# Performance work log

Measured on AMD Instinct MI355X. Metric: run time of the kernel, lower is better.

The kernel has to match this reference:

```python
import jax, jax.numpy as jnp
import numpy as np

N_NODES = 100000
N_EDGES = 1600000
HIDDEN = 128
N_FILTERS = 64
CUTOFF = 8.0
BN_EPS = 1e-3  # keras BatchNormalization default epsilon


def setup_inputs() -> dict:
    key = jax.random.key(0)
    ks = jax.random.split(key, 12)
    x = jax.random.normal(ks[0], (N_NODES, HIDDEN), dtype=jnp.float32)
    edge_index = jax.random.randint(ks[1], (2, N_EDGES), 0, N_NODES, dtype=jnp.int32)
    edge_weight = jax.random.uniform(ks[2], (N_EDGES,), dtype=jnp.float32) * CUTOFF
    edge_attr = jax.random.uniform(ks[3], (N_EDGES, 1), dtype=jnp.float32)
    s = 0.05
    # filter_net: Dense(1->64, tanh), Dense(64->64)
    Wf1 = jax.random.normal(ks[4], (1, N_FILTERS), dtype=jnp.float32) * s
    bf1 = jnp.zeros((N_FILTERS,), jnp.float32)
    Wf2 = jax.random.normal(ks[5], (N_FILTERS, N_FILTERS), dtype=jnp.float32) * s
    bf2 = jnp.zeros((N_FILTERS,), jnp.float32)
    # interaction_net: Dense(128->128, softplus), Dense(128->128)
    Wi1 = jax.random.normal(ks[6], (HIDDEN, HIDDEN), dtype=jnp.float32) * s
    bi1 = jnp.zeros((HIDDEN,), jnp.float32)
    Wi2 = jax.random.normal(ks[7], (HIDDEN, HIDDEN), dtype=jnp.float32) * s
    bi2 = jnp.zeros((HIDDEN,), jnp.float32)
    # BatchNormalization (inference: moving stats)
    gamma = jnp.ones((HIDDEN,), jnp.float32)
    beta = jnp.zeros((HIDDEN,), jnp.float32)
    mov_mean = jax.random.normal(ks[8], (HIDDEN,), dtype=jnp.float32) * 0.01
    mov_var = jnp.ones((HIDDEN,), jnp.float32)
    return {"x": x, "edge_index": edge_index, "edge_weight": edge_weight,
            "edge_attr": edge_attr, "Wf1": Wf1, "bf1": bf1, "Wf2": Wf2, "bf2": bf2,
            "Wi1": Wi1, "bi1": bi1, "Wi2": Wi2, "bi2": bi2,
            "gamma": gamma, "beta": beta, "mov_mean": mov_mean, "mov_var": mov_var}


def reference(x, edge_index, edge_weight, edge_attr, Wf1, bf1, Wf2, bf2,
              Wi1, bi1, Wi2, bi2, gamma, beta, mov_mean, mov_var):
    row, col = edge_index[0], edge_index[1]
    # continuous filters with smooth cosine cutoff
    scaled = edge_weight * (2.0 / CUTOFF) - 1.0                    # [E]
    h = jnp.tanh(scaled[:, None] @ Wf1 + bf1)                      # [E, F]
    filters = h @ Wf2 + bf2                                        # [E, F]
    cut = 0.5 * (jnp.cos(edge_weight * jnp.pi / CUTOFF) + 1.0)
    cut = jnp.where(edge_weight <= CUTOFF, cut, 0.0)               # [E]
    filters = filters * cut[:, None]
    # Original: (neighbor[:, None, :] * filters[:, :, None]).sum(axis=1)
    # == neighbor * filters.sum(-1, keepdims) — same math, no [E,F,H] tensor.
    fsum = jnp.sum(filters, axis=-1, keepdims=True)                # [E, 1]
    messages = x[col] * fsum                                       # [E, H]
    agg = jax.ops.segment_sum(messages, row, num_segments=x.shape[0])  # [N, H]
    out = jax.nn.softplus(agg @ Wi1 + bi1) @ Wi2 + bi2             # [N, H]
    # BatchNormalization, inference mode (training=False)
    out = gamma * (out - mov_mean) * jax.lax.rsqrt(mov_var + BN_EPS) + beta
    return out
```

## Files before the change

### kernel.cpp

```cpp
#include <hip/hip_runtime.h>
#include <math.h>

#define HIDDEN 128
#define NFILT 64
#define SCAN_B 1024
#define LUTK 2048

typedef __attribute__((ext_vector_type(8))) short bf16x8;
typedef __attribute__((ext_vector_type(4))) float f32x4;

__device__ __forceinline__ short f2bf(float f) {
    unsigned u = __float_as_uint(f);
    unsigned r = (u + 0x7fffu + ((u >> 16) & 1u)) >> 16;
    return (short)r;
}
__device__ __forceinline__ float bf2f(unsigned short u) {
    return __uint_as_float(((unsigned)u) << 16);
}

__global__ void wsum_kernel(const float* __restrict__ Wf2, const float* __restrict__ bf2,
                            float* __restrict__ wsum, float* __restrict__ bsum) {
    int j = threadIdx.x;
    float s = 0.f;
    for (int f = 0; f < NFILT; ++f) s += Wf2[j * NFILT + f];
    wsum[j] = s;
    if (j == 0) {
        float b = 0.f;
        for (int f = 0; f < NFILT; ++f) b += bf2[f];
        *bsum = b;
    }
}

__device__ __forceinline__ float edge_coeff(float w,
                                            const float* sW, const float* sB,
                                            const float* sS, float bsum) {
    float s = fmaf(w, 0.25f, -1.0f);
    float acc = bsum;
    #pragma unroll 8
    for (int j = 0; j < NFILT; ++j)
        acc += tanhf(fmaf(s, sW[j], sB[j])) * sS[j];
    float cut = (w <= 8.0f) ? 0.5f * (cosf(w * 0.39269908169872414f) + 1.0f) : 0.0f;
    return acc * cut;
}

__global__ void lut_kernel(const float* __restrict__ Wf1, const float* __restrict__ bf1,
                           const float* __restrict__ wsum, const float* __restrict__ bsum,
                           float* __restrict__ lut) {
    int i = blockIdx.x * 256 + threadIdx.x;
    if (i > LUTK) return;
    float w = 8.0f * (float)i / (float)LUTK;
    lut[i] = edge_coeff(w, Wf1, bf1, wsum, *bsum);
}

__device__ __forceinline__ float lut_eval(const float* sl, float w) {
    float t = w * ((float)LUTK / 8.0f);
    t = fminf(fmaxf(t, 0.f), (float)LUTK);
    int i = (int)t;
    i = min(i, LUTK - 1);
    return fmaf(t - (float)i, sl[i + 1] - sl[i], sl[i]);
}

__global__ void prep_w_kernel(const float* __restrict__ Wi1, const float* __restrict__ Wi2,
                              short* __restrict__ W1T, short* __restrict__ W2T) {
    int idx = blockIdx.x * 256 + threadIdx.x;
    const float* src = (idx < 16384) ? Wi1 : Wi2;
    short* dst = (idx < 16384) ? W1T : W2T;
    int i = idx & 16383;
    int k = i >> 7, n = i & 127;
    dst[n * HIDDEN + k] = f2bf(src[i]);
}

__global__ void prep_bn_kernel(const float* __restrict__ bi2,
                               const float* __restrict__ gamma, const float* __restrict__ beta,
                               const float* __restrict__ mean, const float* __restrict__ var,
                               float* __restrict__ scf, float* __restrict__ shf) {
    int j = threadIdx.x;
    float sc = gamma[j] * rsqrtf(var[j] + 1e-3f);
    scf[j] = sc;
    shf[j] = (bi2[j] - mean[j]) * sc + beta[j];
}

__global__ void x2bf_kernel(const float* __restrict__ x, short* __restrict__ xh, int total8) {
    int i = blockIdx.x * 256 + threadIdx.x;
    if (i >= total8) return;
    const float4 v0 = *(const float4*)&x[(size_t)i * 8];
    const float4 v1 = *(const float4*)&x[(size_t)i * 8 + 4];
    bf16x8 o;
    o[0] = f2bf(v0.x); o[1] = f2bf(v0.y); o[2] = f2bf(v0.z); o[3] = f2bf(v0.w);
    o[4] = f2bf(v1.x); o[5] = f2bf(v1.y); o[6] = f2bf(v1.z); o[7] = f2bf(v1.w);
    *(bf16x8*)&xh[(size_t)i * 8] = o;
}

__global__ void count_rank_kernel(const int* __restrict__ rows, int* __restrict__ deg,
                                  int* __restrict__ rank, int E) {
    int e = blockIdx.x * blockDim.x + threadIdx.x;
    if (e < E) rank[e] = atomicAdd(&deg[rows[e]], 1);
}

__global__ void count_kernel(const int* __restrict__ rows, int* __restrict__ deg, int E) {
    int e = blockIdx.x * blockDim.x + threadIdx.x;
    if (e < E) atomicAdd(&deg[rows[e]], 1);
}

__global__ __launch_bounds__(SCAN_B) void scan_p1(const int* __restrict__ deg,
                                                  int* __restrict__ bsums, int N) {
    __shared__ int red[SCAN_B];
    int i = blockIdx.x * SCAN_B + threadIdx.x;
    red[threadIdx.x] = (i < N) ? deg[i] : 0;
    __syncthreads();
    for (int off = SCAN_B / 2; off > 0; off >>= 1) {
        if (threadIdx.x < off) red[threadIdx.x] += red[threadIdx.x + off];
        __syncthreads();
    }
    if (threadIdx.x == 0) bsums[blockIdx.x] = red[0];
}

__global__ __launch_bounds__(SCAN_B) void scan_p2(int* __restrict__ bsums, int B) {
    __shared__ int part[SCAN_B];
    int t = threadIdx.x;
    part[t] = (t < B) ? bsums[t] : 0;
    __syncthreads();
    for (int off = 1; off < SCAN_B; off <<= 1) {
        int v = (t >= off) ? part[t - off] : 0;
        __syncthreads();
        part[t] += v;
        __syncthreads();
    }
    if (t < B) bsums[t] = (t == 0) ? 0 : part[t - 1];
}

template <bool WRITE_CURSOR>
__global__ __launch_bounds__(SCAN_B) void scan_p3_t(int* __restrict__ deg,
                                                    const int* __restrict__ bsums,
                                                    int* __restrict__ offs, int N) {
    __shared__ int part[SCAN_B];
    int t = threadIdx.x;
    int i = blockIdx.x * SCAN_B + t;
    int d = (i < N) ? deg[i] : 0;
    part[t] = d;
    __syncthreads();
    for (int off = 1; off < SCAN_B; off <<= 1) {
        int v = (t >= off) ? part[t - off] : 0;
        __syncthreads();
        part[t] += v;
        __syncthreads();
    }
    int pre = bsums[blockIdx.x] + part[t] - d;
    if (i < N) {
        offs[i] = pre;
        if (WRITE_CURSOR) deg[i] = pre;
        if (i == N - 1) offs[N] = pre + d;
    }
}

__global__ __launch_bounds__(256) void fill_rank_kernel(
    const int* __restrict__ rows, const int* __restrict__ cols,
    const float* __restrict__ ew, const int* __restrict__ rank,
    const int* __restrict__ offs, const float* __restrict__ lut,
    int2* __restrict__ epack, int E) {
    __shared__ float sl[LUTK + 1];
    for (int i = threadIdx.x; i <= LUTK; i += 256) sl[i] = lut[i];
    __syncthreads();
    int e = blockIdx.x * 256 + threadIdx.x;
    if (e >= E) return;
    float f = lut_eval(sl, ew[e]);
    int pos = offs[rows[e]] + rank[e];
    epack[pos] = make_int2(cols[e], __float_as_int(f));
}

__global__ __launch_bounds__(256) void fill_cursor_kernel(
    const int* __restrict__ rows, const int* __restrict__ cols,
    const float* __restrict__ ew, int* __restrict__ cursor,
    const float* __restrict__ lut, int2* __restrict__ epack, int E) {
    __shared__ float sl[LUTK + 1];
    for (int i = threadIdx.x; i <= LUTK; i += 256) sl[i] = lut[i];
    __syncthreads();
    int e = blockIdx.x * 256 + threadIdx.x;
    if (e >= E) return;
    float f = lut_eval(sl, ew[e]);
    int pos = atomicAdd(&cursor[rows[e]], 1);
    epack[pos] = make_int2(cols[e], __float_as_int(f));
}

__global__ __launch_bounds__(256) void gather_bf_kernel(const int* __restrict__ offs,
                                                        const int2* __restrict__ epack,
                                                        const short* __restrict__ xh,
                                                        short* __restrict__ aggh, int N) {
    int t = threadIdx.x;
    int node = blockIdx.x * 8 + (t >> 5);
    if (node >= N) return;
    int lane = t & 31;
    int s = offs[node], eend = offs[node + 1];
    float a0 = 0.f, a1 = 0.f, a2 = 0.f, a3 = 0.f;

    int i = s;
    for (; i + 4 <= eend; i += 4) {
        int2 p0 = epack[i];
        int2 p1 = epack[i + 1];
        int2 p2 = epack[i + 2];
        int2 p3 = epack[i + 3];
        ushort4 x0 = *(const ushort4*)&xh[(size_t)p0.x * HIDDEN + lane * 4];
        ushort4 x1 = *(const ushort4*)&xh[(size_t)p1.x * HIDDEN + lane * 4];
        ushort4 x2 = *(const ushort4*)&xh[(size_t)p2.x * HIDDEN + lane * 4];
        ushort4 x3 = *(const ushort4*)&xh[(size_t)p3.x * HIDDEN + lane * 4];
        float f0 = __int_as_float(p0.y), f1 = __int_as_float(p1.y);
        float f2 = __int_as_float(p2.y), f3 = __int_as_float(p3.y);
        a0 = fmaf(bf2f(x0.x), f0, a0); a1 = fmaf(bf2f(x0.y), f0, a1);
        a2 = fmaf(bf2f(x0.z), f0, a2); a3 = fmaf(bf2f(x0.w), f0, a3);
        a0 = fmaf(bf2f(x1.x), f1, a0); a1 = fmaf(bf2f(x1.y), f1, a1);
        a2 = fmaf(bf2f(x1.z), f1, a2); a3 = fmaf(bf2f(x1.w), f1, a3);
        a0 = fmaf(bf2f(x2.x), f2, a0); a1 = fmaf(bf2f(x2.y), f2, a1);
        a2 = fmaf(bf2f(x2.z), f2, a2); a3 = fmaf(bf2f(x2.w), f2, a3);
        a0 = fmaf(bf2f(x3.x), f3, a0); a1 = fmaf(bf2f(x3.y), f3, a1);
        a2 = fmaf(bf2f(x3.z), f3, a2); a3 = fmaf(bf2f(x3.w), f3, a3);
    }
    for (; i < eend; ++i) {
        int2 p = epack[i];
        float f = __int_as_float(p.y);
        ushort4 xv = *(const ushort4*)&xh[(size_t)p.x * HIDDEN + lane * 4];
        a0 = fmaf(bf2f(xv.x), f, a0);
        a1 = fmaf(bf2f(xv.y), f, a1);
        a2 = fmaf(bf2f(xv.z), f, a2);
        a3 = fmaf(bf2f(xv.w), f, a3);
    }
    ushort4 o;
    o.x = (unsigned short)f2bf(a0);
    o.y = (unsigned short)f2bf(a1);
    o.z = (unsigned short)f2bf(a2);
    o.w = (unsigned short)f2bf(a3);
    *(ushort4*)&aggh[(size_t)node * HIDDEN + lane * 4] = o;
}

__global__ __launch_bounds__(256) void gather_kernel(const int* __restrict__ offs,
                                                     const int2* __restrict__ epack,
                                                     const float* __restrict__ x,
                                                     float* __restrict__ agg, int N) {
    int t = threadIdx.x;
    int node = blockIdx.x * 8 + (t >> 5);
    if (node >= N) return;
    int lane = t & 31;
    int s = offs[node], eend = offs[node + 1];
    float4 acc = make_float4(0.f, 0.f, 0.f, 0.f);
    int i = s;
    for (; i + 2 <= eend; i += 2) {
        int2 p0 = epack[i];
        int2 p1 = epack[i + 1];
        float4 x0 = *(const float4*)&x[(size_t)p0.x * HIDDEN + lane * 4];
        float4 x1 = *(const float4*)&x[(size_t)p1.x * HIDDEN + lane * 4];
        float f0 = __int_as_float(p0.y), f1 = __int_as_float(p1.y);
        acc.x = fmaf(x0.x, f0, acc.x); acc.y = fmaf(x0.y, f0, acc.y);
        acc.z = fmaf(x0.z, f0, acc.z); acc.w = fmaf(x0.w, f0, acc.w);
        acc.x = fmaf(x1.x, f1, acc.x); acc.y = fmaf(x1.y, f1, acc.y);
        acc.z = fmaf(x1.z, f1, acc.z); acc.w = fmaf(x1.w, f1, acc.w);
    }
    for (; i < eend; ++i) {
        int2 p = epack[i];
        float f = __int_as_float(p.y);
        const float4 xv = *(const float4*)&x[(size_t)p.x * HIDDEN + lane * 4];
        acc.x = fmaf(xv.x, f, acc.x);
        acc.y = fmaf(xv.y, f, acc.y);
        acc.z = fmaf(xv.z, f, acc.z);
        acc.w = fmaf(xv.w, f, acc.w);
    }
    *(float4*)&agg[(size_t)node * HIDDEN + lane * 4] = acc;
}

#define HROW 136

__global__ __launch_bounds__(256) void mlp_mfma_bf_kernel(
    const short* __restrict__ aggh, float* __restrict__ io,
    const short* __restrict__ W1T, const short* __restrict__ W2T,
    const float* __restrict__ bi1,
    const float* __restrict__ scf, const float* __restrict__ shf,
    int N) {
    __shared__ short hS[64 * HROW];

    const int t = threadIdx.x;
    const int wave = t >> 6;
    const int lane = t & 63;
    const int quad = lane >> 4;
    const int m16  = lane & 15;
    const int row0 = blockIdx.x * 64 + wave * 16;
    const int arow = row0 + m16;

    f32x4 acc[8];
    #pragma unroll
    for (int ct = 0; ct < 8; ++ct) acc[ct] = (f32x4)(0.f);

    #pragma unroll
    for (int ks = 0; ks < 4; ++ks) {
        bf16x8 a;
        if (arow < N) {
            a = *(const bf16x8*)&aggh[(size_t)arow * HIDDEN + ks * 32 + quad * 8];
        } else {
            #pragma unroll
            for (int j = 0; j < 8; ++j) a[j] = 0;
        }
        #pragma unroll
        for (int ct = 0; ct < 8; ++ct) {
            bf16x8 b = *(const bf16x8*)&W1T[(ct * 16 + m16) * HIDDEN + ks * 32 + quad * 8];
            acc[ct] = __builtin_amdgcn_mfma_f32_16x16x32_bf16(a, b, acc[ct], 0, 0, 0);
        }
    }

    #pragma unroll
    for (int ct = 0; ct < 8; ++ct) {
        int col = ct * 16 + m16;
        float b1 = bi1[col];
        #pragma unroll
        for (int r = 0; r < 4; ++r) {
            int lrow = wave * 16 + quad * 4 + r;
            float v = acc[ct][r] + b1;
            float h = (v > 20.f) ? v : log1pf(__expf(v));
            hS[lrow * HROW + col] = f2bf(h);
            acc[ct][r] = 0.f;
        }
    }
    __syncthreads();

    #pragma unroll
    for (int ks = 0; ks < 4; ++ks) {
        bf16x8 a = *(const bf16x8*)&hS[(wave * 16 + m16) * HROW + ks * 32 + quad * 8];
        #pragma unroll
        for (int ct = 0; ct < 8; ++ct) {
            bf16x8 b = *(const bf16x8*)&W2T[(ct * 16 + m16) * HIDDEN + ks * 32 + quad * 8];
            acc[ct] = __builtin_amdgcn_mfma_f32_16x16x32_bf16(a, b, acc[ct], 0, 0, 0);
        }
    }

    #pragma unroll
    for (int ct = 0; ct < 8; ++ct) {
        int col = ct * 16 + m16;
        float sc = scf[col], sh = shf[col];
        #pragma unroll
        for (int r = 0; r < 4; ++r) {
            int grow = row0 + quad * 4 + r;
            if (grow < N)
                io[(size_t)grow * HIDDEN + col] = fmaf(acc[ct][r], sc, sh);
        }
    }
}

__global__ __launch_bounds__(256) void mlp_mfma_kernel(
    float* io,
    const short* __restrict__ W1T, const short* __restrict__ W2T,
    const float* __restrict__ bi1,
    const float* __restrict__ scf, const float* __restrict__ shf,
    int N) {
    __shared__ short hS[64 * HROW];

    const int t = threadIdx.x;
    const int wave = t >> 6;
    const int lane = t & 63;
    const int quad = lane >> 4;
    const int m16  = lane & 15;
    const int row0 = blockIdx.x * 64 + wave * 16;
    const int arow = row0 + m16;

    f32x4 acc[8];
    #pragma unroll
    for (int ct = 0; ct < 8; ++ct) acc[ct] = (f32x4)(0.f);

    #pragma unroll
    for (int ks = 0; ks < 4; ++ks) {
        bf16x8 a;
        if (arow < N) {
            const float* ap = &io[(size_t)arow * HIDDEN + ks * 32 + quad * 8];
            float4 v0 = *(const float4*)ap;
            float4 v1 = *(const float4*)(ap + 4);
            a[0] = f2bf(v0.x); a[1] = f2bf(v0.y); a[2] = f2bf(v0.z); a[3] = f2bf(v0.w);
            a[4] = f2bf(v1.x); a[5] = f2bf(v1.y); a[6] = f2bf(v1.z); a[7] = f2bf(v1.w);
        } else {
            #pragma unroll
            for (int j = 0; j < 8; ++j) a[j] = 0;
        }
        #pragma unroll
        for (int ct = 0; ct < 8; ++ct) {
            bf16x8 b = *(const bf16x8*)&W1T[(ct * 16 + m16) * HIDDEN + ks * 32 + quad * 8];
            acc[ct] = __builtin_amdgcn_mfma_f32_16x16x32_bf16(a, b, acc[ct], 0, 0, 0);
        }
    }

    #pragma unroll
    for (int ct = 0; ct < 8; ++ct) {
        int col = ct * 16 + m16;
        float b1 = bi1[col];
        #pragma unroll
        for (int r = 0; r < 4; ++r) {
            int lrow = wave * 16 + quad * 4 + r;
            float v = acc[ct][r] + b1;
            float h = (v > 20.f) ? v : log1pf(__expf(v));
            hS[lrow * HROW + col] = f2bf(h);
            acc[ct][r] = 0.f;
        }
    }
    __syncthreads();

    #pragma unroll
    for (int ks = 0; ks < 4; ++ks) {
        bf16x8 a = *(const bf16x8*)&hS[(wave * 16 + m16) * HROW + ks * 32 + quad * 8];
        #pragma unroll
        for (int ct = 0; ct < 8; ++ct) {
            bf16x8 b = *(const bf16x8*)&W2T[(ct * 16 + m16) * HIDDEN + ks * 32 + quad * 8];
            acc[ct] = __builtin_amdgcn_mfma_f32_16x16x32_bf16(a, b, acc[ct], 0, 0, 0);
        }
    }

    #pragma unroll
    for (int ct = 0; ct < 8; ++ct) {
        int col = ct * 16 + m16;
        float sc = scf[col], sh = shf[col];
        #pragma unroll
        for (int r = 0; r < 4; ++r) {
            int grow = row0 + quad * 4 + r;
            if (grow < N)
                io[(size_t)grow * HIDDEN + col] = fmaf(acc[ct][r], sc, sh);
        }
    }
}

__global__ void edge_filter_kernel(const float* __restrict__ ew,
                                   const float* __restrict__ Wf1, const float* __restrict__ bf1,
                                   const float* __restrict__ wsum, const float* __restrict__ bsum,
                                   float* __restrict__ fs, int E) {
    __shared__ float sW[NFILT], sB[NFILT], sS[NFILT];
    if (threadIdx.x < NFILT) {
        sW[threadIdx.x] = Wf1[threadIdx.x];
        sB[threadIdx.x] = bf1[threadIdx.x];
        sS[threadIdx.x] = wsum[threadIdx.x];
    }
    __syncthreads();
    int e = blockIdx.x * blockDim.x + threadIdx.x;
    if (e >= E) return;
    fs[e] = edge_coeff(ew[e], sW, sB, sS, *bsum);
}

__global__ void scatter_kernel(const int* __restrict__ rows, const int* __restrict__ cols,
                               const float* __restrict__ x, const float* __restrict__ fs,
                               float* __restrict__ agg, int E) {
    int t = threadIdx.x;
    int e = blockIdx.x * 8 + (t >> 5);
    if (e >= E) return;
    int lane = t & 31;
    int r = rows[e];
    int c = cols[e];
    float f = fs[e];
    const float4 xv = *(const float4*)&x[c * HIDDEN + lane * 4];
    float* dst = &agg[r * HIDDEN + lane * 4];
    atomicAdd(dst + 0, xv.x * f);
    atomicAdd(dst + 1, xv.y * f);
    atomicAdd(dst + 2, xv.z * f);
    atomicAdd(dst + 3, xv.w * f);
}

__global__ __launch_bounds__(256) void mlp_kernel(
    float* __restrict__ io,
    const float* __restrict__ Wi1, const float* __restrict__ bi1,
    const float* __restrict__ Wi2, const float* __restrict__ bi2,
    const float* __restrict__ gamma, const float* __restrict__ beta,
    const float* __restrict__ mean, const float* __restrict__ var,
    int N) {
    __shared__ float As[64 * HIDDEN];
    __shared__ float Wh[64 * HIDDEN];

    const int t = threadIdx.x;
    const int row0 = blockIdx.x * 64;
    const int col4 = (t & 31) * 4;
    const int rgrp = t >> 5;

    #pragma unroll
    for (int i = 0; i < 8; ++i) {
        int f4 = t + 256 * i;
        int r = f4 >> 5, c4 = (f4 & 31) * 4;
        int node = row0 + r;
        float4 v = make_float4(0.f, 0.f, 0.f, 0.f);
        if (node < N) v = *(const float4*)&io[node * HIDDEN + c4];
        *(float4*)&As[r * HIDDEN + c4] = v;
    }

    float acc[8][4];
    #pragma unroll
    for (int r = 0; r < 8; ++r)
        for (int j = 0; j < 4; ++j) acc[r][j] = 0.f;

    for (int kh = 0; kh < 2; ++kh) {
        __syncthreads();
        #pragma unroll
        for (int i = 0; i < 8; ++i) {
            int f4 = t + 256 * i;
            int kr = f4 >> 5, c4 = (f4 & 31) * 4;
            *(float4*)&Wh[kr * HIDDEN + c4] = *(const float4*)&Wi1[(kh * 64 + kr) * HIDDEN + c4];
        }
        __syncthreads();
        for (int k = 0; k < 64; ++k) {
            float4 w = *(const float4*)&Wh[k * HIDDEN + col4];
            #pragma unroll
            for (int r = 0; r < 8; ++r) {
                float a = As[(rgrp + 8 * r) * HIDDEN + kh * 64 + k];
                acc[r][0] = fmaf(a, w.x, acc[r][0]);
                acc[r][1] = fmaf(a, w.y, acc[r][1]);
                acc[r][2] = fmaf(a, w.z, acc[r][2]);
                acc[r][3] = fmaf(a, w.w, acc[r][3]);
            }
        }
    }
    __syncthreads();

    {
        float4 b = *(const float4*)&bi1[col4];
        float bv[4] = {b.x, b.y, b.z, b.w};
        #pragma unroll
        for (int r = 0; r < 8; ++r) {
            float hv[4];
            #pragma unroll
            for (int j = 0; j < 4; ++j) {
                float v = acc[r][j] + bv[j];
                hv[j] = (v > 20.f) ? v : log1pf(__expf(v));
                acc[r][j] = 0.f;
            }
            *(float4*)&As[(rgrp + 8 * r) * HIDDEN + col4] =
                make_float4(hv[0], hv[1], hv[2], hv[3]);
        }
    }

    for (int kh = 0; kh < 2; ++kh) {
        __syncthreads();
        #pragma unroll
        for (int i = 0; i < 8; ++i) {
            int f4 = t + 256 * i;
            int kr = f4 >> 5, c4 = (f4 & 31) * 4;
            *(float4*)&Wh[kr * HIDDEN + c4] = *(const float4*)&Wi2[(kh * 64 + kr) * HIDDEN + c4];
        }
        __syncthreads();
        for (int k = 0; k < 64; ++k) {
            float4 w = *(const float4*)&Wh[k * HIDDEN + col4];
            #pragma unroll
            for (int r = 0; r < 8; ++r) {
                float a = As[(rgrp + 8 * r) * HIDDEN + kh * 64 + k];
                acc[r][0] = fmaf(a, w.x, acc[r][0]);
                acc[r][1] = fmaf(a, w.y, acc[r][1]);
                acc[r][2] = fmaf(a, w.z, acc[r][2]);
                acc[r][3] = fmaf(a, w.w, acc[r][3]);
            }
        }
    }

    {
        float4 b2 = *(const float4*)&bi2[col4];
        float4 g  = *(const float4*)&gamma[col4];
        float4 be = *(const float4*)&beta[col4];
        float4 mu = *(const float4*)&mean[col4];
        float4 va = *(const float4*)&var[col4];
        float bv[4]  = {b2.x, b2.y, b2.z, b2.w};
        float gv[4]  = {g.x, g.y, g.z, g.w};
        float bev[4] = {be.x, be.y, be.z, be.w};
        float muv[4] = {mu.x, mu.y, mu.z, mu.w};
        float vav[4] = {va.x, va.y, va.z, va.w};
        float sc[4];
        #pragma unroll
        for (int j = 0; j < 4; ++j) sc[j] = gv[j] * rsqrtf(vav[j] + 1e-3f);
        #pragma unroll
        for (int r = 0; r < 8; ++r) {
            int node = row0 + rgrp + 8 * r;
            if (node < N) {
                float o[4];
                #pragma unroll
                for (int j = 0; j < 4; ++j)
                    o[j] = (acc[r][j] + bv[j] - muv[j]) * sc[j] + bev[j];
                *(float4*)&io[node * HIDDEN + col4] = make_float4(o[0], o[1], o[2], o[3]);
            }
        }
    }
}

extern "C" void kernel_launch(void* const* d_in, const int* in_sizes, int n_in,
                              void* d_out, int out_size, void* d_ws, size_t ws_size,
                              hipStream_t stream) {
    const float* x    = (const float*)d_in[0];
    const int*   ei   = (const int*)d_in[1];
    const float* ew   = (const float*)d_in[2];
    const float* Wf1  = (const float*)d_in[4];
    const float* bf1  = (const float*)d_in[5];
    const float* Wf2  = (const float*)d_in[6];
    const float* bf2  = (const float*)d_in[7];
    const float* Wi1  = (const float*)d_in[8];
    const float* bi1  = (const float*)d_in[9];
    const float* Wi2  = (const float*)d_in[10];
    const float* bi2  = (const float*)d_in[11];
    const float* gam  = (const float*)d_in[12];
    const float* bet  = (const float*)d_in[13];
    const float* mmu  = (const float*)d_in[14];
    const float* mva  = (const float*)d_in[15];

    const int N = in_sizes[0] / HIDDEN;
    const int E = in_sizes[2];
    const int* rows = ei;
    const int* cols = ei + E;

    float* io = (float*)d_out;

    const int B = (N + SCAN_B - 1) / SCAN_B;

    char* ws = (char*)d_ws;
    int*   deg    = (int*)ws;
    int*   offs   = deg + N;
    int*   bsums  = offs + N + 1;
    float* wsumv  = (float*)(bsums + B);
    float* bsumv  = wsumv + NFILT;
    float* lut    = bsumv + 1;
    size_t hdr_ints  = (size_t)(2 * N + 1 + B + NFILT + 1 + LUTK + 1);
    size_t epack_off = ((hdr_ints * 4) + 15) & ~(size_t)15;
    int2*  epack  = (int2*)(ws + epack_off);
    size_t wT_off = (epack_off + (size_t)E * sizeof(int2) + 15) & ~(size_t)15;
    short* W1T    = (short*)(ws + wT_off);
    short* W2T    = W1T + HIDDEN * HIDDEN;
    float* scf    = (float*)(W2T + HIDDEN * HIDDEN);
    float* shf    = scf + HIDDEN;
    size_t base_need = wT_off + 2 * HIDDEN * HIDDEN * sizeof(short) + 2 * HIDDEN * sizeof(float);
    size_t rank_off  = (base_need + 15) & ~(size_t)15;
    int*   rank   = (int*)(ws + rank_off);
    size_t rank_need = rank_off + (size_t)E * sizeof(int);
    size_t xh_off    = (rank_need + 15) & ~(size_t)15;
    short* xh     = (short*)(ws + xh_off);
    short* aggh   = xh + (size_t)N * HIDDEN;
    size_t bf_need = xh_off + 2 * (size_t)N * HIDDEN * sizeof(short);

    if (ws_size >= base_need && B <= SCAN_B) {
        const bool use_rank = (ws_size >= rank_need);
        const bool use_bf   = (ws_size >= bf_need);
        hipMemsetAsync(deg, 0, (size_t)N * sizeof(int), stream);
        wsum_kernel<<<1, 64, 0, stream>>>(Wf2, bf2, wsumv, bsumv);
        lut_kernel<<<(LUTK + 256) / 256, 256, 0, stream>>>(Wf1, bf1, wsumv, bsumv, lut);
        prep_w_kernel<<<128, 256, 0, stream>>>(Wi1, Wi2, W1T, W2T);
        prep_bn_kernel<<<1, HIDDEN, 0, stream>>>(bi2, gam, bet, mmu, mva, scf, shf);
        if (use_bf) {
            int total8 = N * (HIDDEN / 8);
            x2bf_kernel<<<(total8 + 255) / 256, 256, 0, stream>>>(x, xh, total8);
        }
        if (use_rank)
            count_rank_kernel<<<(E + 255) / 256, 256, 0, stream>>>(rows, deg, rank, E);
        else
            count_kernel<<<(E + 255) / 256, 256, 0, stream>>>(rows, deg, E);
        scan_p1<<<B, SCAN_B, 0, stream>>>(deg, bsums, N);
        scan_p2<<<1, SCAN_B, 0, stream>>>(bsums, B);
        if (use_rank) {
            scan_p3_t<false><<<B, SCAN_B, 0, stream>>>(deg, bsums, offs, N);
            fill_rank_kernel<<<(E + 255) / 256, 256, 0, stream>>>(rows, cols, ew, rank,
                                                                  offs, lut, epack, E);
        } else {
            scan_p3_t<true><<<B, SCAN_B, 0, stream>>>(deg, bsums, offs, N);
            fill_cursor_kernel<<<(E + 255) / 256, 256, 0, stream>>>(rows, cols, ew, deg,
                                                                    lut, epack, E);
        }
        if (use_bf) {
            gather_bf_kernel<<<(N + 7) / 8, 256, 0, stream>>>(offs, epack, xh, aggh, N);
            mlp_mfma_bf_kernel<<<(N + 63) / 64, 256, 0, stream>>>(aggh, io, W1T, W2T,
                                                                  bi1, scf, shf, N);
        } else {
            gather_kernel<<<(N + 7) / 8, 256, 0, stream>>>(offs, epack, x, io, N);
            mlp_mfma_kernel<<<(N + 63) / 64, 256, 0, stream>>>(io, W1T, W2T, bi1, scf, shf, N);
        }
    } else {
        float* fs = (float*)d_ws;
        float* w2 = fs + E;
        float* b2 = w2 + NFILT;
        hipMemsetAsync(d_out, 0, (size_t)out_size * sizeof(float), stream);
        wsum_kernel<<<1, 64, 0, stream>>>(Wf2, bf2, w2, b2);
        edge_filter_kernel<<<(E + 255) / 256, 256, 0, stream>>>(ew, Wf1, bf1, w2, b2, fs, E);
        scatter_kernel<<<(E + 7) / 8, 256, 0, stream>>>(rows, cols, x, fs, io, E);
        mlp_kernel<<<(N + 63) / 64, 256, 0, stream>>>(io, Wi1, bi1, Wi2, bi2,
                                                      gam, bet, mmu, mva, N);
    }
}
```

Baseline: 427.7 us.

## Stage MLP weights in swizzled LDS, enlarge block, use fast softplus

The bf16 MFMA MLP kernel now loads W1 and W2 into shared memory with an XOR swizzle instead of having every wave read the B fragments from global memory. The block grows to 512 threads covering 128 rows so each weight load serves more rows. Softplus is computed with hardware exp2/log intrinsics instead of log1pf/expf, and bias, scale and shift are hoisted into registers. This trades extra LDS use and barriers, plus slightly lower softplus precision, for fewer global weight reads and cheaper transcendentals.

```diff
diff --git a/kernel.cpp b/kernel.cpp
--- a/kernel.cpp
+++ b/kernel.cpp
@@ -16,6 +16,12 @@
 }
 __device__ __forceinline__ float bf2f(unsigned short u) {
     return __uint_as_float(((unsigned)u) << 16);
+}
+
+__device__ __forceinline__ float softplus_fast(float v) {
+    float e = __builtin_amdgcn_exp2f(v * 1.4426950408889634f);
+    float r = 0.69314718055994531f * __builtin_amdgcn_logf(1.0f + e);
+    return (v > 80.f) ? v : r;
 }
 
 __global__ void wsum_kernel(const float* __restrict__ Wf2, const float* __restrict__ bf2,
@@ -267,25 +273,52 @@
 
 #define HROW 136
 
-__global__ __launch_bounds__(256) void mlp_mfma_bf_kernel(
+#define WSWZ(b) ((b) ^ ((((b) >> 8) & 7) << 4))
+
+__global__ __launch_bounds__(512) void mlp_mfma_bf_kernel(
     const short* __restrict__ aggh, float* __restrict__ io,
     const short* __restrict__ W1T, const short* __restrict__ W2T,
     const float* __restrict__ bi1,
     const float* __restrict__ scf, const float* __restrict__ shf,
     int N) {
-    __shared__ short hS[64 * HROW];
+    __shared__ short wS[HIDDEN * HIDDEN];
+    __shared__ short hS[128 * HROW];
 
     const int t = threadIdx.x;
     const int wave = t >> 6;
     const int lane = t & 63;
     const int quad = lane >> 4;
     const int m16  = lane & 15;
-    const int row0 = blockIdx.x * 64 + wave * 16;
+    const int row0 = blockIdx.x * 128 + wave * 16;
     const int arow = row0 + m16;
 
+    const int swzmask = (m16 & 7) << 4;
+
+    bf16x8 w2r[4];
+    {
+        const bf16x8* w1v = (const bf16x8*)W1T;
+        const bf16x8* w2v = (const bf16x8*)W2T;
+        bf16x8 w1r[4];
+        #pragma unroll
+        for (int j = 0; j < 4; ++j) w1r[j] = w1v[t + 512 * j];
+        #pragma unroll
+        for (int j = 0; j < 4; ++j) w2r[j] = w2v[t + 512 * j];
+        #pragma unroll
+        for (int j = 0; j < 4; ++j) {
+            int b = (t + 512 * j) * 16;
+            *(bf16x8*)((char*)wS + WSWZ(b)) = w1r[j];
+        }
+    }
+
+    float b1v[8];
+    #pragma unroll
+    for (int ct = 0; ct < 8; ++ct) b1v[ct] = bi1[ct * 16 + m16];
+
     f32x4 acc[8];
     #pragma unroll
     for (int ct = 0; ct < 8; ++ct) acc[ct] = (f32x4)(0.f);
+
+    __syncthreads();
 
     #pragma unroll
     for (int ks = 0; ks < 4; ++ks) {
@@ -296,9 +329,10 @@
             #pragma unroll
             for (int j = 0; j < 8; ++j) a[j] = 0;
         }
+        const char* bbase = (const char*)wS + m16 * 256 + ((ks * 64 + quad * 16) ^ swzmask);
         #pragma unroll
         for (int ct = 0; ct < 8; ++ct) {
-            bf16x8 b = *(const bf16x8*)&W1T[(ct * 16 + m16) * HIDDEN + ks * 32 + quad * 8];
+            bf16x8 b = *(const bf16x8*)(bbase + ct * 4096);
             acc[ct] = __builtin_amdgcn_mfma_f32_16x16x32_bf16(a, b, acc[ct], 0, 0, 0);
         }
     }
@@ -306,37 +340,49 @@
     #pragma unroll
     for (int ct = 0; ct < 8; ++ct) {
         int col = ct * 16 + m16;
-        float b1 = bi1[col];
         #pragma unroll
         for (int r = 0; r < 4; ++r) {
             int lrow = wave * 16 + quad * 4 + r;
-            float v = acc[ct][r] + b1;
-            float h = (v > 20.f) ? v : log1pf(__expf(v));
+            float h = softplus_fast(acc[ct][r] + b1v[ct]);
             hS[lrow * HROW + col] = f2bf(h);
-            acc[ct][r] = 0.f;
-        }
-    }
-    __syncthreads();
+        }
+        acc[ct] = (f32x4)(0.f);
+    }
+    __syncthreads();
+
+    #pragma unroll
+    for (int j = 0; j < 4; ++j) {
+        int b = (t + 512 * j) * 16;
+        *(bf16x8*)((char*)wS + WSWZ(b)) = w2r[j];
+    }
+    __syncthreads();
+
+    float scv[8], shv[8];
+    #pragma unroll
+    for (int ct = 0; ct < 8; ++ct) {
+        scv[ct] = scf[ct * 16 + m16];
+        shv[ct] = shf[ct * 16 + m16];
+    }
 
     #pragma unroll
     for (int ks = 0; ks < 4; ++ks) {
         bf16x8 a = *(const bf16x8*)&hS[(wave * 16 + m16) * HROW + ks * 32 + quad * 8];
+        const char* bbase = (const char*)wS + m16 * 256 + ((ks * 64 + quad * 16) ^ swzmask);
         #pragma unroll
         for (int ct = 0; ct < 8; ++ct) {
-            bf16x8 b = *(const bf16x8*)&W2T[(ct * 16 + m16) * HIDDEN + ks * 32 + quad * 8];
+            bf16x8 b = *(const bf16x8*)(bbase + ct * 4096);
             acc[ct] = __builtin_amdgcn_mfma_f32_16x16x32_bf16(a, b, acc[ct], 0, 0, 0);
         }
     }
 
     #pragma unroll
-    for (int ct = 0; ct < 8; ++ct) {
-        int col = ct * 16 + m16;
-        float sc = scf[col], sh = shf[col];
-        #pragma unroll
-        for (int r = 0; r < 4; ++r) {
-            int grow = row0 + quad * 4 + r;
-            if (grow < N)
-                io[(size_t)grow * HIDDEN + col] = fmaf(acc[ct][r], sc, sh);
+    for (int r = 0; r < 4; ++r) {
+        int grow = row0 + quad * 4 + r;
+        if (grow < N) {
+            float* p = &io[(size_t)grow * HIDDEN + m16];
+            #pragma unroll
+            for (int ct = 0; ct < 8; ++ct)
+                p[ct * 16] = fmaf(acc[ct][r], scv[ct], shv[ct]);
         }
     }
 }
@@ -388,8 +434,7 @@
         #pragma unroll
         for (int r = 0; r < 4; ++r) {
             int lrow = wave * 16 + quad * 4 + r;
-            float v = acc[ct][r] + b1;
-            float h = (v > 20.f) ? v : log1pf(__expf(v));
+            float h = softplus_fast(acc[ct][r] + b1);
             hS[lrow * HROW + col] = f2bf(h);
             acc[ct][r] = 0.f;
         }
@@ -515,7 +560,7 @@
             #pragma unroll
             for (int j = 0; j < 4; ++j) {
                 float v = acc[r][j] + bv[j];
-                hv[j] = (v > 20.f) ? v : log1pf(__expf(v));
+                hv[j] = softplus_fast(v);
                 acc[r][j] = 0.f;
             }
             *(float4*)&As[(rgrp + 8 * r) * HIDDEN + col4] =
@@ -654,8 +699,8 @@
         }
         if (use_bf) {
             gather_bf_kernel<<<(N + 7) / 8, 256, 0, stream>>>(offs, epack, xh, aggh, N);
-            mlp_mfma_bf_kernel<<<(N + 63) / 64, 256, 0, stream>>>(aggh, io, W1T, W2T,
-                                                                  bi1, scf, shf, N);
+            mlp_mfma_bf_kernel<<<(N + 127) / 128, 512, 0, stream>>>(aggh, io, W1T, W2T,
+                                                                    bi1, scf, shf, N);
         } else {
             gather_kernel<<<(N + 7) / 8, 256, 0, stream>>>(offs, epack, x, io, N);
             mlp_mfma_kernel<<<(N + 63) / 64, 256, 0, stream>>>(io, W1T, W2T, bi1, scf, shf, N);
```

After: 367.4 us. 1.16x faster.
